# Kernel tuning notes

Hardware: AMD Instinct MI355X
Metric: run time of the kernel (lower is better)

The kernel has to match this reference:

```python
import jax, jax.numpy as jnp
import numpy as np

N_USER = 100000
N_ITEM = 100000
E_USER = 3200000
E_ITEM = 3200000
RANK = 10
N_CONV = 32
ORD = 5
N_ITER = 10
BATCH = 65536
R_MIN = 1.0
R_RANGE = 4.0


def _spmm(row, col, val, X, n):
    # sparse COO matmul: (sum_j A[i,j] X[j]) via gather + segment_sum
    return jax.ops.segment_sum(val[:, None] * X[col], row, num_segments=n)


def _cheb_conv(row, col, val, n, X, Wc, bc, K):
    # normalized graph Laplacian L = I - D^-1/2 A D^-1/2, Chebyshev terms T_k(L) X
    deg = jax.ops.segment_sum(val, row, num_segments=n)
    dinv = jnp.where(deg > 0, deg ** -0.5, 0.0)

    def L(Y):
        return Y - dinv[:, None] * _spmm(row, col, val, dinv[:, None] * Y, n)

    Ts = [X]
    if K > 1:
        Ts.append(L(X))
    for _ in range(2, K):
        Ts.append(2.0 * L(Ts[-1]) - Ts[-2])
    feat = jnp.concatenate(Ts, axis=1)  # [n, K*rank]
    return jax.nn.relu(feat @ Wc + bc)  # [n, n_conv_feat]


def _lstm(x, h, c, Wg, Ug, bg):
    # gates stacked as [4, F, F] in order (f, i, o, update); note the source
    # uses sigmoid for the cell-update and h = o * sigmoid(c) (faithful).
    g = jax.nn.sigmoid(jnp.einsum('nf,kfo->kno', x, Wg)
                       + jnp.einsum('nf,kfo->kno', h, Ug)
                       + bg[:, None, :])
    f, i, o, u = g[0], g[1], g[2], g[3]
    c = f * c + i * u
    h = o * jax.nn.sigmoid(c)
    return h, c


def setup_inputs() -> dict:
    key = jax.random.key(0)
    ks = jax.random.split(key, 24)
    f32 = jnp.float32

    def gl(k, shape, scale):
        return jax.random.normal(k, shape, dtype=f32) * scale

    inp = {
        'user_id': jax.random.randint(ks[0], (BATCH,), 0, N_USER),
        'item_id': jax.random.randint(ks[1], (BATCH,), 0, N_ITEM),
        'ug_row': jax.random.randint(ks[2], (E_USER,), 0, N_USER),
        'ug_col': jax.random.randint(ks[3], (E_USER,), 0, N_USER),
        'ug_val': jax.random.uniform(ks[4], (E_USER,), dtype=f32),
        'ig_row': jax.random.randint(ks[5], (E_ITEM,), 0, N_ITEM),
        'ig_col': jax.random.randint(ks[6], (E_ITEM,), 0, N_ITEM),
        'ig_val': jax.random.uniform(ks[7], (E_ITEM,), dtype=f32),
        'W0': gl(ks[8], (N_USER, RANK), 0.1),
        'H0': gl(ks[9], (N_ITEM, RANK), 0.1),
        'W_conv_W': gl(ks[10], (ORD * RANK, N_CONV), (ORD * RANK) ** -0.5),
        'b_conv_W': jnp.zeros((N_CONV,), f32),
        'W_conv_H': gl(ks[11], (ORD * RANK, N_CONV), (ORD * RANK) ** -0.5),
        'b_conv_H': jnp.zeros((N_CONV,), f32),
        'Wg_u': gl(ks[12], (4, N_CONV, N_CONV), N_CONV ** -0.5),
        'Ug_u': gl(ks[13], (4, N_CONV, N_CONV), N_CONV ** -0.5),
        'bg_u': jnp.zeros((4, N_CONV), f32),
        'Wg_m': gl(ks[14], (4, N_CONV, N_CONV), N_CONV ** -0.5),
        'Ug_m': gl(ks[15], (4, N_CONV, N_CONV), N_CONV ** -0.5),
        'bg_m': jnp.zeros((4, N_CONV), f32),
        'W_out_W': gl(ks[16], (N_CONV, RANK), N_CONV ** -0.5),
        'b_out_W': jnp.zeros((RANK,), f32),
        'W_out_H': gl(ks[17], (N_CONV, RANK), N_CONV ** -0.5),
        'b_out_H': jnp.zeros((RANK,), f32),
    }
    return inp


def reference(user_id, item_id, ug_row, ug_col, ug_val, ig_row, ig_col, ig_val,
              W0, H0, W_conv_W, b_conv_W, W_conv_H, b_conv_H,
              Wg_u, Ug_u, bg_u, Wg_m, Ug_m, bg_m,
              W_out_W, b_out_W, W_out_H, b_out_H):
    nu, ni = W0.shape[0], H0.shape[0]
    F = Wg_u.shape[1]
    W, H = W0, H0
    h_u = jnp.zeros((nu, F), W0.dtype)
    c_u = jnp.zeros((nu, F), W0.dtype)
    h_m = jnp.zeros((ni, F), H0.dtype)
    c_m = jnp.zeros((ni, F), H0.dtype)

    for _ in range(N_ITER):
        xu = _cheb_conv(ug_row, ug_col, ug_val, nu, W, W_conv_W, b_conv_W, ORD)
        xm = _cheb_conv(ig_row, ig_col, ig_val, ni, H, W_conv_H, b_conv_H, ORD)
        h_u, c_u = _lstm(xu, h_u, c_u, Wg_u, Ug_u, bg_u)
        h_m, c_m = _lstm(xm, h_m, c_m, Wg_m, Ug_m, bg_m)
        W = W + jnp.tanh(h_u @ W_out_W + b_out_W)
        H = H + jnp.tanh(h_m @ W_out_H + b_out_H)

    r = jnp.sum(W[user_id] * H[item_id], axis=1)  # [batch]
    return R_MIN + R_RANGE * jax.nn.sigmoid(r)
```

## Files before the change

kernel.cpp:

```cpp
#include <hip/hip_runtime.h>
#include <hip/hip_fp16.h>
#include <cstdint>

typedef unsigned short u16;
typedef unsigned int u32;
typedef unsigned long long u64;

#define NN 100000
#define EE 3200000
constexpr int GS = 100032;

constexpr size_t OFF_CNTDEG = 0;
constexpr size_t OFF_DBIN   = OFF_CNTDEG + (size_t)2 * GS * 8;
constexpr size_t OFF_RPS    = OFF_DBIN + 12288;
constexpr size_t OFF_FILL   = OFF_RPS + (size_t)2 * GS * 4;
constexpr size_t OFF_PERM   = OFF_FILL + (size_t)2 * GS * 4;
constexpr size_t OFF_ISLOT  = OFF_PERM + (size_t)2 * GS * 4;
constexpr size_t OFF_DINV   = OFF_ISLOT + (size_t)2 * GS * 4;
constexpr int WTOTAL = 20564;
constexpr size_t OFF_WTS    = OFF_DINV + (size_t)2 * GS * 4;
constexpr size_t WTS_PAD    = (((size_t)WTOTAL * 4 + 63) / 64) * 64;
constexpr size_t OFF_W      = OFF_WTS + WTS_PAD;
constexpr size_t OFF_ZI     = OFF_W + (size_t)2 * NN * 12 * 4;
constexpr size_t OFF_FEAT   = OFF_ZI + (size_t)2 * 2 * NN * 32;
constexpr size_t OFF_H      = OFF_FEAT + (size_t)2 * NN * 60 * 4;
constexpr size_t OFF_C      = OFF_H + (size_t)2 * NN * 32 * 4;
constexpr size_t OFF_CE     = OFF_C + (size_t)2 * NN * 32 * 4;
constexpr size_t WS_NEED    = OFF_CE + (size_t)2 * EE * 4;

constexpr int WOFF_WCW = 0, WOFF_BCW = 1600, WOFF_WCH = 1632, WOFF_BCH = 3232;
constexpr int WOFF_WGU = 3264, WOFF_UGU = 7360, WOFF_BGU = 11456;
constexpr int WOFF_WGM = 11584, WOFF_UGM = 15680, WOFF_BGM = 19776;
constexpr int WOFF_WOW = 19904, WOFF_BOW = 20224, WOFF_WOH = 20234, WOFF_BOH = 20554;

constexpr int NBPG = (NN + 255) / 256;

__device__ __forceinline__ float sigf(float x) { return 1.f / (1.f + __expf(-x)); }
__device__ __forceinline__ float ldf(const void* p, long long i, int bf) {
  if (bf) return __uint_as_float(((u32)((const u16*)p)[i]) << 16);
  return ((const float*)p)[i];
}
__device__ __forceinline__ u16 f2b(float f) {
  u32 u = __float_as_uint(f);
  return (u16)((u + 0x7FFFu + ((u >> 16) & 1u)) >> 16);
}
__device__ __forceinline__ float h_lo(u32 u) { return __half2float(__ushort_as_half((u16)u)); }
__device__ __forceinline__ float h_hi(u32 u) { return __half2float(__ushort_as_half((u16)(u >> 16))); }
__device__ __forceinline__ float h_15(u32 u) { return __half2float(__ushort_as_half((u16)(u & 0x7FFFu))); }
__device__ __forceinline__ u32 pk_h2(float a, float b) {
  return (u32)__half_as_ushort(__float2half(a)) | ((u32)__half_as_ushort(__float2half(b)) << 16);
}
__device__ __forceinline__ void z_write(u32* zbuf, int row, const float* v) {
  u32* zr = zbuf + (size_t)row * 8;
  *(uint4*)zr = make_uint4(pk_h2(v[0], v[1]), pk_h2(v[2], v[3]), pk_h2(v[4], v[5]), pk_h2(v[6], v[7]));
  zr[4] = pk_h2(v[8], v[9]);
}

__global__ __launch_bounds__(256) void k_detect(const u16* __restrict__ uv, u32* __restrict__ flag) {
  int t = threadIdx.x;
  u32 any = 0;
  for (int j = t; j < 8192; j += 256) any |= (uv[j] & 0x8000u);
  unsigned long long b = __ballot(any != 0);
  if (t == 0) flag[0] = (b == 0ull) ? 1u : 0u;
}

__global__ __launch_bounds__(256) void k_init(const void* __restrict__ W0, const void* __restrict__ H0,
                                              float* __restrict__ W, const u32* __restrict__ flag) {
  int t = blockIdx.x * 256 + threadIdx.x;
  if (t >= 2 * NN) return;
  int bf = flag[0];
  int g = (t >= NN) ? 1 : 0;
  int n = t - g * NN;
  const void* src = g ? H0 : W0;
  float* dst = W + ((size_t)g * NN + n) * 12;
#pragma unroll
  for (int r = 0; r < 10; r++) dst[r] = ldf(src, (long long)n * 10 + r, bf);
  dst[10] = 0.f; dst[11] = 0.f;
}

__global__ __launch_bounds__(256) void k_hist(const int* __restrict__ ur, const void* __restrict__ uv,
                                              const int* __restrict__ ir, const void* __restrict__ iv,
                                              u64* __restrict__ cntdeg, const u32* __restrict__ flag) {
  int bf = flag[0];
  long long stride = (long long)gridDim.x * blockDim.x;
  for (long long t = (long long)blockIdx.x * blockDim.x + threadIdx.x; t < 2LL * EE; t += stride) {
    int g = (t >= EE) ? 1 : 0;
    int e = (int)(t - (long long)g * EE);
    int row = (g ? ir : ur)[e];
    float v = ldf(g ? iv : uv, e, bf);
    u64 pack = (1ull << 40) | (u64)(u32)(v * 67108864.f + 0.5f);
    atomicAdd(&cntdeg[(size_t)g * GS + row], pack);
  }
}

__global__ __launch_bounds__(256) void k_dcount(const u64* __restrict__ cntdeg, u32* __restrict__ dbin) {
  __shared__ u32 lh[512];
  int tid = threadIdx.x;
  lh[tid] = 0; lh[tid + 256] = 0;
  __syncthreads();
  int t = blockIdx.x * 256 + tid;
  if (t < 2 * NN) {
    int g = (t >= NN) ? 1 : 0;
    int n = t - g * NN;
    u32 cnt = (u32)(cntdeg[(size_t)g * GS + n] >> 40);
    u32 d = cnt > 255u ? 255u : cnt;
    atomicAdd(&lh[g * 256 + d], 1u);
  }
  __syncthreads();
  if (lh[tid]) atomicAdd(&dbin[tid], lh[tid]);
  if (lh[tid + 256]) atomicAdd(&dbin[tid + 256], lh[tid + 256]);
}

__global__ __launch_bounds__(512) void k_dscan(const u32* __restrict__ dbin, u32* __restrict__ doff) {
  __shared__ u32 sh[512];
  int t = threadIdx.x;
  u32 own = dbin[t];
  sh[t] = own;
  __syncthreads();
  for (int off = 1; off < 256; off <<= 1) {
    u32 v = ((t & 255) >= off) ? sh[t - off] : 0;
    __syncthreads();
    sh[t] += v;
    __syncthreads();
  }
  doff[t] = sh[t] - own;
}

__global__ __launch_bounds__(256) void k_dplace(const u64* __restrict__ cntdeg, const u32* __restrict__ doff,
                                                u32* __restrict__ dfill, int* __restrict__ perm,
                                                int* __restrict__ islot, float* __restrict__ dinv) {
  int t = blockIdx.x * 256 + threadIdx.x;
  if (t >= 2 * NN) return;
  int g = (t >= NN) ? 1 : 0;
  int n = t - g * NN;
  u64 u = cntdeg[(size_t)g * GS + n];
  u32 cnt = (u32)(u >> 40);
  u32 d = cnt > 255u ? 255u : cnt;
  u32 pos = doff[g * 256 + d] + atomicAdd(&dfill[g * 256 + d], 1u);
  perm[(size_t)g * GS + pos] = n;
  islot[(size_t)g * GS + n] = (int)pos;
  u64 dfx = u & 0xFFFFFFFFFFull;
  dinv[(size_t)g * GS + n] = dfx ? rsqrtf((float)dfx * (1.f / 67108864.f)) : 0.f;
}

__global__ __launch_bounds__(256) void k_scan1(const u64* __restrict__ cntdeg, const int* __restrict__ perm,
                                               int* __restrict__ rps, int* __restrict__ bsum) {
  int g = (blockIdx.x >= NBPG) ? 1 : 0;
  int b = blockIdx.x - g * NBPG;
  int tid = threadIdx.x;
  int i = b * 256 + tid;
  int c = 0;
  if (i < NN) c = (int)(cntdeg[(size_t)g * GS + perm[(size_t)g * GS + i]] >> 40);
  __shared__ int sh[256];
  sh[tid] = c;
  __syncthreads();
  for (int off = 1; off < 256; off <<= 1) {
    int v = (tid >= off) ? sh[tid - off] : 0;
    __syncthreads();
    sh[tid] += v;
    __syncthreads();
  }
  int incl = sh[tid];
  if (i < NN) rps[(size_t)g * GS + i] = incl - c;
  if (tid == 255) bsum[g * 512 + b] = incl;
}

__global__ __launch_bounds__(512) void k_scan2(int* __restrict__ bsum) {
  int g = blockIdx.x;
  int t = threadIdx.x;
  __shared__ int sh[512];
  int v = (t < NBPG) ? bsum[g * 512 + t] : 0;
  int own = v;
  sh[t] = v;
  __syncthreads();
  for (int off = 1; off < 512; off <<= 1) {
    int u2 = (t >= off) ? sh[t - off] : 0;
    __syncthreads();
    sh[t] += u2;
    __syncthreads();
  }
  if (t < NBPG) bsum[g * 512 + t] = sh[t] - own;
}

__global__ __launch_bounds__(256) void k_scan3(int* __restrict__ rps, int* __restrict__ fill,
                                               const int* __restrict__ bsum) {
  int g = (blockIdx.x >= NBPG) ? 1 : 0;
  int b = blockIdx.x - g * NBPG;
  int i = b * 256 + threadIdx.x;
  if (i < NN) {
    int v = rps[(size_t)g * GS + i] + bsum[g * 512 + b];
    rps[(size_t)g * GS + i] = v;
    fill[(size_t)g * GS + i] = v;
  }
  if (b == 0 && threadIdx.x == 0) rps[(size_t)g * GS + NN] = EE;
}

__global__ __launch_bounds__(256) void k_scatter(const int* __restrict__ ur, const int* __restrict__ uc,
                                                 const void* __restrict__ uv, const int* __restrict__ ir,
                                                 const int* __restrict__ ic, const void* __restrict__ iv,
                                                 const int* __restrict__ islot, int* __restrict__ fill,
                                                 u32* __restrict__ ce, const u32* __restrict__ flag) {
  int bf = flag[0];
  long long stride = (long long)gridDim.x * blockDim.x;
  for (long long t = (long long)blockIdx.x * blockDim.x + threadIdx.x; t < 2LL * EE; t += stride) {
    int g = (t >= EE) ? 1 : 0;
    int e = (int)(t - (long long)g * EE);
    int row = (g ? ir : ur)[e];
    int col = (g ? ic : uc)[e];
    float v = ldf(g ? iv : uv, e, bf);
    int sl = islot[(size_t)g * GS + row];
    int pos = atomicAdd(&fill[(size_t)g * GS + sl], 1);
    ce[(size_t)g * EE + pos] = ((u32)col << 15) | (u32)__half_as_ushort(__float2half(v));
  }
}

struct P14 { const void* p[14]; };
__global__ __launch_bounds__(256) void k_cvtw(P14 w, float* __restrict__ dst, const u32* __restrict__ flag) {
  int t = blockIdx.x * 256 + threadIdx.x;
  if (t >= WTOTAL) return;
  int bf = flag[0];
  const int sz[14] = {1600, 32, 1600, 32, 4096, 4096, 128, 4096, 4096, 128, 320, 10, 320, 10};
  int off = 0;
#pragma unroll
  for (int s = 0; s < 14; s++) {
    if (t < off + sz[s]) { dst[t] = ldf(w.p[s], t - off, bf); return; }
    off += sz[s];
  }
}

__global__ __launch_bounds__(256) void k_prep(const float* __restrict__ W, const int* __restrict__ perm,
                                              const float* __restrict__ dinv, float* __restrict__ feat,
                                              u32* __restrict__ Z) {
  int t = blockIdx.x * 256 + threadIdx.x;
  if (t >= 2 * NN) return;
  int g = (t >= NN) ? 1 : 0;
  int slot = t - g * NN;
  int row = perm[(size_t)g * GS + slot];
  float dv = dinv[(size_t)g * GS + row];
  const float* w = W + ((size_t)g * NN + row) * 12;
  float* f = feat + ((size_t)g * NN + slot) * 60;
  float zv[10];
#pragma unroll
  for (int r = 0; r < 10; r++) { float x = w[r]; f[r] = x; zv[r] = dv * x; }
  z_write(Z + ((size_t)g * 2 + 0) * NN * 8, row, zv);
}

template <int K>
__global__ __launch_bounds__(256) void k_cheb(const int* __restrict__ rps, const u32* __restrict__ ce,
                                              const int* __restrict__ perm, const float* __restrict__ dinv,
                                              float* __restrict__ feat, u32* __restrict__ Z) {
  constexpr int NBG = NN / 32;
  int x = blockIdx.x;
  int xcd = x & 7;
  int g = xcd >> 2;
  int b = (x >> 3) * 4 + (xcd & 3);
  if (b >= NBG) return;
  int tid = threadIdx.x;
  int r = tid & 7;
  int slot = b * 32 + (tid >> 3);
  const u32* Zin = Z + (((size_t)g * 2 + ((K - 1) & 1)) * NN) * 8;
  const int* rp = rps + (size_t)g * GS;
  int e0 = rp[slot];
  int e1 = rp[slot + 1];
  const u32* cep = ce + (size_t)g * EE;
  float acc0 = 0.f, acc1 = 0.f;
#pragma unroll 4
  for (int e = e0; e < e1; ++e) {
    u32 ec = cep[e];
    u32 col = ec >> 15;
    float c = h_15(ec);
    u32 zw = Zin[(size_t)col * 8 + r];
    acc0 += c * h_lo(zw);
    acc1 += c * h_hi(zw);
  }
  if (r < 5) {
    int row = perm[(size_t)g * GS + slot];
    float dv = dinv[(size_t)g * GS + row];
    float* frow = feat + ((size_t)g * NN + slot) * 60;
    float2 tp = *(const float2*)(frow + (K - 1) * 12 + 2 * r);
    float tv0 = tp.x - dv * acc0;
    float tv1 = tp.y - dv * acc1;
    if constexpr (K >= 2) {
      float2 t2 = *(const float2*)(frow + (K - 2) * 12 + 2 * r);
      tv0 = 2.f * tv0 - t2.x;
      tv1 = 2.f * tv1 - t2.y;
    }
    *(float2*)(frow + K * 12 + 2 * r) = make_float2(tv0, tv1);
    if constexpr (K < 4) {
      u32* Zout = Z + (((size_t)g * 2 + (K & 1)) * NN) * 8;
      Zout[(size_t)row * 8 + r] = pk_h2(dv * tv0, dv * tv1);
    }
  }
}

__global__ __launch_bounds__(256) void k_convlstm(const float* __restrict__ feat_c, float* __restrict__ H,
                                                  float* __restrict__ C, float* __restrict__ W,
                                                  const int* __restrict__ perm, const float* __restrict__ dinv,
                                                  float* __restrict__ feat, u32* __restrict__ Z,
                                                  const float* __restrict__ wts) {
  constexpr int NB = (NN + 255) / 256;
  int g = (blockIdx.x >= NB) ? 1 : 0;
  int n = (blockIdx.x - g * NB) * 256 + threadIdx.x;
  __shared__ float sigi[256 * 33];
  if (n >= NN) return;
  const float* Wc = wts + (g ? WOFF_WCH : WOFF_WCW);
  const float* bc = wts + (g ? WOFF_BCH : WOFF_BCW);
  const float* Wg = wts + (g ? WOFF_WGM : WOFF_WGU);
  const float* Ug = wts + (g ? WOFF_UGM : WOFF_UGU);
  const float* bg = wts + (g ? WOFF_BGM : WOFF_BGU);
  const float* Wo = wts + (g ? WOFF_WOH : WOFF_WOW);
  const float* bo = wts + (g ? WOFF_BOH : WOFF_BOW);
  const float* frow_c = feat_c + ((size_t)g * NN + n) * 60;
  float xr[32];
#pragma unroll
  for (int o = 0; o < 32; o++) xr[o] = bc[o];
#pragma unroll
  for (int k = 0; k < 5; k++) {
    const float4* f4 = (const float4*)(frow_c + k * 12);
    float4 a = f4[0], b2 = f4[1], c2 = f4[2];
    float fv[10] = {a.x, a.y, a.z, a.w, b2.x, b2.y, b2.z, b2.w, c2.x, c2.y};
#pragma unroll
    for (int j = 0; j < 10; j++) {
      const float* wr = Wc + (k * 10 + j) * 32;
      float xv = fv[j];
#pragma unroll
      for (int o = 0; o < 32; o++) xr[o] += xv * wr[o];
    }
  }
#pragma unroll
  for (int o = 0; o < 32; o++) xr[o] = fmaxf(xr[o], 0.f);
  float* hp = H + ((size_t)g * NN + n) * 32;
  float* cp = C + ((size_t)g * NN + n) * 32;
  float hr[32], cr[32];
#pragma unroll
  for (int o = 0; o < 32; o += 4) {
    *(float4*)(hr + o) = *(const float4*)(hp + o);
    *(float4*)(cr + o) = *(const float4*)(cp + o);
  }
  float* si = &sigi[threadIdx.x * 33];
#pragma unroll 1
  for (int kk = 0; kk < 4; kk++) {
    int k = (kk == 0) ? 0 : (kk == 1) ? 1 : (kk == 2) ? 3 : 2;
    const float* wgk = Wg + k * 1024;
    const float* ugk = Ug + k * 1024;
    const float* bgk = bg + k * 32;
    float acc[32];
#pragma unroll
    for (int o = 0; o < 32; o++) acc[o] = bgk[o];
#pragma unroll
    for (int f = 0; f < 32; f++) {
      float xv = xr[f];
      const float* w = wgk + f * 32;
#pragma unroll
      for (int o = 0; o < 32; o++) acc[o] += xv * w[o];
    }
#pragma unroll
    for (int f = 0; f < 32; f++) {
      float hv = hr[f];
      const float* w = ugk + f * 32;
#pragma unroll
      for (int o = 0; o < 32; o++) acc[o] += hv * w[o];
    }
#pragma unroll
    for (int o = 0; o < 32; o++) acc[o] = sigf(acc[o]);
    if (kk == 0) {
#pragma unroll
      for (int o = 0; o < 32; o++) cr[o] *= acc[o];
    } else if (kk == 1) {
#pragma unroll
      for (int o = 0; o < 32; o++) si[o] = acc[o];
    } else if (kk == 2) {
#pragma unroll
      for (int o = 0; o < 32; o++) cr[o] += si[o] * acc[o];
    } else {
#pragma unroll
      for (int o = 0; o < 32; o++) hr[o] = acc[o] * sigf(cr[o]);
    }
  }
#pragma unroll
  for (int o = 0; o < 32; o += 4) {
    *(float4*)(hp + o) = *(float4*)(hr + o);
    *(float4*)(cp + o) = *(float4*)(cr + o);
  }
  float aw[10];
#pragma unroll
  for (int r = 0; r < 10; r++) aw[r] = bo[r];
#pragma unroll
  for (int f = 0; f < 32; f++) {
    float hv = hr[f];
    const float* w = Wo + f * 10;
#pragma unroll
    for (int r = 0; r < 10; r++) aw[r] += hv * w[r];
  }
  int row = perm[(size_t)g * GS + n];
  float dv = dinv[(size_t)g * GS + row];
  float* wrow = W + ((size_t)g * NN + row) * 12;
  float* frow = feat + ((size_t)g * NN + n) * 60;
  float zv[10];
#pragma unroll
  for (int r = 0; r < 10; r++) {
    float t = fminf(fmaxf(aw[r], -15.f), 15.f);
    float e = __expf(2.f * t);
    float th = (e - 1.f) / (e + 1.f);
    float wn = wrow[r] + th;
    wrow[r] = wn;
    frow[r] = wn;
    zv[r] = dv * wn;
  }
  z_write(Z + ((size_t)g * 2 + 0) * NN * 8, row, zv);
}

__global__ __launch_bounds__(256) void k_score(const int* __restrict__ uid, const int* __restrict__ iid,
                                               const float* __restrict__ W, void* __restrict__ outp,
                                               const u32* __restrict__ flag) {
  int t = blockIdx.x * 256 + threadIdx.x;
  if (t >= 65536) return;
  int u = uid[t], i = iid[t];
  const float* wr = W + (size_t)u * 12;
  const float* hr = W + ((size_t)NN + i) * 12;
  float r = 0.f;
#pragma unroll
  for (int k = 0; k < 10; k++) r += wr[k] * hr[k];
  float v = 1.f + 4.f * sigf(r);
  if (flag[0]) ((u16*)outp)[t] = f2b(v);
  else         ((float*)outp)[t] = v;
}

extern "C" void kernel_launch(void* const* d_in, const int* in_sizes, int n_in,
                              void* d_out, int out_size, void* d_ws, size_t ws_size,
                              hipStream_t stream) {
  (void)in_sizes; (void)n_in; (void)out_size;
  if (ws_size < WS_NEED) return;

  const int* uid = (const int*)d_in[0];
  const int* iid = (const int*)d_in[1];
  const int* ur = (const int*)d_in[2];
  const int* uc = (const int*)d_in[3];
  const void* uv = d_in[4];
  const int* ir = (const int*)d_in[5];
  const int* ic = (const int*)d_in[6];
  const void* iv = d_in[7];

  char* ws = (char*)d_ws;
  u64* cntdeg = (u64*)(ws + OFF_CNTDEG);
  u32* dbin = (u32*)(ws + OFF_DBIN);
  u32* dfill = dbin + 512;
  u32* doff = dbin + 1024;
  int* bsum = (int*)(dbin + 1536);
  u32* flag = dbin + 2560;
  int* rps = (int*)(ws + OFF_RPS);
  int* fill = (int*)(ws + OFF_FILL);
  int* perm = (int*)(ws + OFF_PERM);
  int* islot = (int*)(ws + OFF_ISLOT);
  float* dinv = (float*)(ws + OFF_DINV);
  float* wts = (float*)(ws + OFF_WTS);
  float* W = (float*)(ws + OFF_W);
  u32* Z = (u32*)(ws + OFF_ZI);
  float* feat = (float*)(ws + OFF_FEAT);
  float* H = (float*)(ws + OFF_H);
  float* C = (float*)(ws + OFF_C);
  u32* ce = (u32*)(ws + OFF_CE);

  hipMemsetAsync(ws, 0, OFF_DBIN + 4096, stream);
  hipMemsetAsync(ws + OFF_H, 0, (size_t)4 * NN * 32 * 4, stream);

  k_detect<<<1, 256, 0, stream>>>((const u16*)uv, flag);
  k_init<<<(2 * NN + 255) / 256, 256, 0, stream>>>(d_in[8], d_in[9], W, flag);
  k_hist<<<4096, 256, 0, stream>>>(ur, uv, ir, iv, cntdeg, flag);
  k_dcount<<<(2 * NN + 255) / 256, 256, 0, stream>>>(cntdeg, dbin);
  k_dscan<<<1, 512, 0, stream>>>(dbin, doff);
  k_dplace<<<(2 * NN + 255) / 256, 256, 0, stream>>>(cntdeg, doff, dfill, perm, islot, dinv);
  k_scan1<<<2 * NBPG, 256, 0, stream>>>(cntdeg, perm, rps, bsum);
  k_scan2<<<2, 512, 0, stream>>>(bsum);
  k_scan3<<<2 * NBPG, 256, 0, stream>>>(rps, fill, bsum);
  k_scatter<<<4096, 256, 0, stream>>>(ur, uc, uv, ir, ic, iv, islot, fill, ce, flag);
  P14 wp;
  for (int i = 0; i < 14; i++) wp.p[i] = d_in[10 + i];
  k_cvtw<<<(WTOTAL + 255) / 256, 256, 0, stream>>>(wp, wts, flag);
  k_prep<<<(2 * NN + 255) / 256, 256, 0, stream>>>(W, perm, dinv, feat, Z);

  constexpr int NBG = NN / 32;
  constexpr int CHEB_GRID = 8 * ((NBG + 3) / 4);
  constexpr int NODE_GRID = 2 * ((NN + 255) / 256);
  for (int it = 0; it < 10; ++it) {
    k_cheb<1><<<CHEB_GRID, 256, 0, stream>>>(rps, ce, perm, dinv, feat, Z);
    k_cheb<2><<<CHEB_GRID, 256, 0, stream>>>(rps, ce, perm, dinv, feat, Z);
    k_cheb<3><<<CHEB_GRID, 256, 0, stream>>>(rps, ce, perm, dinv, feat, Z);
    k_cheb<4><<<CHEB_GRID, 256, 0, stream>>>(rps, ce, perm, dinv, feat, Z);
    k_convlstm<<<NODE_GRID, 256, 0, stream>>>(feat, H, C, W, perm, dinv, feat, Z, wts);
  }
  k_score<<<256, 256, 0, stream>>>(uid, iid, W, d_out, flag);
}
```

Baseline: 5.522 ms.

## Pad CSR rows to multiples of eight for vectorized edge loads in Chebyshev SpMM

Rounds each row's edge count up to a multiple of eight in the row-pointer scan and zero-fills the padded edge array, so the SpMM inner loop can read edges with two 128-bit loads and issue eight independent gathers per step. Zero padding entries point at column 0 with zero weight and contribute nothing. Gathers of Z now use nontemporal loads. The cost is extra padded work (about 3.5 elements per row), a larger edge buffer and one additional memset.

```diff
diff --git a/kernel.cpp b/kernel.cpp
--- a/kernel.cpp
+++ b/kernel.cpp
@@ -9,6 +9,7 @@
 #define NN 100000
 #define EE 3200000
 constexpr int GS = 100032;
+constexpr int CEPG = EE + 700000;
 
 constexpr size_t OFF_CNTDEG = 0;
 constexpr size_t OFF_DBIN   = OFF_CNTDEG + (size_t)2 * GS * 8;
@@ -26,7 +27,7 @@
 constexpr size_t OFF_H      = OFF_FEAT + (size_t)2 * NN * 60 * 4;
 constexpr size_t OFF_C      = OFF_H + (size_t)2 * NN * 32 * 4;
 constexpr size_t OFF_CE     = OFF_C + (size_t)2 * NN * 32 * 4;
-constexpr size_t WS_NEED    = OFF_CE + (size_t)2 * EE * 4;
+constexpr size_t WS_NEED    = OFF_CE + (size_t)2 * CEPG * 4;
 
 constexpr int WOFF_WCW = 0, WOFF_BCW = 1600, WOFF_WCH = 1632, WOFF_BCH = 3232;
 constexpr int WOFF_WGU = 3264, WOFF_UGU = 7360, WOFF_BGU = 11456;
@@ -150,7 +151,10 @@
   int tid = threadIdx.x;
   int i = b * 256 + tid;
   int c = 0;
-  if (i < NN) c = (int)(cntdeg[(size_t)g * GS + perm[(size_t)g * GS + i]] >> 40);
+  if (i < NN) {
+    u32 cnt = (u32)(cntdeg[(size_t)g * GS + perm[(size_t)g * GS + i]] >> 40);
+    c = (int)((cnt + 7u) & ~7u);
+  }
   __shared__ int sh[256];
   sh[tid] = c;
   __syncthreads();
@@ -165,7 +169,7 @@
   if (tid == 255) bsum[g * 512 + b] = incl;
 }
 
-__global__ __launch_bounds__(512) void k_scan2(int* __restrict__ bsum) {
+__global__ __launch_bounds__(512) void k_scan2(int* __restrict__ bsum, int* __restrict__ rps) {
   int g = blockIdx.x;
   int t = threadIdx.x;
   __shared__ int sh[512];
@@ -180,6 +184,7 @@
     __syncthreads();
   }
   if (t < NBPG) bsum[g * 512 + t] = sh[t] - own;
+  if (t == NBPG - 1) rps[(size_t)g * GS + NN] = sh[t];
 }
 
 __global__ __launch_bounds__(256) void k_scan3(int* __restrict__ rps, int* __restrict__ fill,
@@ -192,7 +197,6 @@
     rps[(size_t)g * GS + i] = v;
     fill[(size_t)g * GS + i] = v;
   }
-  if (b == 0 && threadIdx.x == 0) rps[(size_t)g * GS + NN] = EE;
 }
 
 __global__ __launch_bounds__(256) void k_scatter(const int* __restrict__ ur, const int* __restrict__ uc,
@@ -210,7 +214,7 @@
     float v = ldf(g ? iv : uv, e, bf);
     int sl = islot[(size_t)g * GS + row];
     int pos = atomicAdd(&fill[(size_t)g * GS + sl], 1);
-    ce[(size_t)g * EE + pos] = ((u32)col << 15) | (u32)__half_as_ushort(__float2half(v));
+    ce[(size_t)g * CEPG + pos] = ((u32)col << 15) | (u32)__half_as_ushort(__float2half(v));
   }
 }
 
@@ -262,16 +266,22 @@
   const int* rp = rps + (size_t)g * GS;
   int e0 = rp[slot];
   int e1 = rp[slot + 1];
-  const u32* cep = ce + (size_t)g * EE;
+  const u32* cep = ce + (size_t)g * CEPG;
   float acc0 = 0.f, acc1 = 0.f;
-#pragma unroll 4
-  for (int e = e0; e < e1; ++e) {
-    u32 ec = cep[e];
-    u32 col = ec >> 15;
-    float c = h_15(ec);
-    u32 zw = Zin[(size_t)col * 8 + r];
-    acc0 += c * h_lo(zw);
-    acc1 += c * h_hi(zw);
+  for (int e = e0; e < e1; e += 8) {
+    uint4 ca = *(const uint4*)(cep + e);
+    uint4 cb = *(const uint4*)(cep + e + 4);
+    u32 ecs[8] = {ca.x, ca.y, ca.z, ca.w, cb.x, cb.y, cb.z, cb.w};
+    u32 zw[8];
+#pragma unroll
+    for (int j = 0; j < 8; j++)
+      zw[j] = __builtin_nontemporal_load(Zin + (size_t)(ecs[j] >> 15) * 8 + r);
+#pragma unroll
+    for (int j = 0; j < 8; j++) {
+      float c = h_15(ecs[j]);
+      acc0 += c * h_lo(zw[j]);
+      acc1 += c * h_hi(zw[j]);
+    }
   }
   if (r < 5) {
     int row = perm[(size_t)g * GS + slot];
@@ -463,6 +473,7 @@
 
   hipMemsetAsync(ws, 0, OFF_DBIN + 4096, stream);
   hipMemsetAsync(ws + OFF_H, 0, (size_t)4 * NN * 32 * 4, stream);
+  hipMemsetAsync(ce, 0, (size_t)2 * CEPG * 4, stream);
 
   k_detect<<<1, 256, 0, stream>>>((const u16*)uv, flag);
   k_init<<<(2 * NN + 255) / 256, 256, 0, stream>>>(d_in[8], d_in[9], W, flag);
@@ -471,7 +482,7 @@
   k_dscan<<<1, 512, 0, stream>>>(dbin, doff);
   k_dplace<<<(2 * NN + 255) / 256, 256, 0, stream>>>(cntdeg, doff, dfill, perm, islot, dinv);
   k_scan1<<<2 * NBPG, 256, 0, stream>>>(cntdeg, perm, rps, bsum);
-  k_scan2<<<2, 512, 0, stream>>>(bsum);
+  k_scan2<<<2, 512, 0, stream>>>(bsum, rps);
   k_scan3<<<2 * NBPG, 256, 0, stream>>>(rps, fill, bsum);
   k_scatter<<<4096, 256, 0, stream>>>(ur, uc, uv, ir, ic, iv, islot, fill, ce, flag);
   P14 wp;
```

Measured after the change: 7.924 ms. 1.44x slower.
